# Kernel optimization log

Measured on AMD Instinct MI355X. Metric: run time of the kernel, lower is better.

## Reference

```python
import jax, jax.numpy as jnp
import numpy as np

BASIS_ORDER = 7  # basis_dim = 8 (Chebyshev T_0..T_7 of tanh(x))


def chebyshev_basis(x, order=BASIS_ORDER):
    """x: [batch, in] -> [batch, in, order+1] Chebyshev basis on tanh(x)."""
    xt = jnp.tanh(x)
    terms = [jnp.ones_like(xt), xt]
    for _ in range(2, order + 1):
        terms.append(2.0 * xt * terms[-1] - terms[-2])
    return jnp.stack(terms[: order + 1], axis=-1)


def setup_inputs() -> dict:
    key = jax.random.key(0)
    k1, k2, k3 = jax.random.split(key, 3)
    batch, in_f, out_f, K = 4096, 1024, 1024, BASIS_ORDER + 1
    x = jax.random.normal(k1, (batch, in_f), dtype=jnp.float32)
    # Kaiming-uniform-ish init scale
    bound = 1.0 / np.sqrt(in_f * K)
    weights = jax.random.uniform(k2, (out_f, in_f, K), dtype=jnp.float32,
                                 minval=-bound, maxval=bound)
    bias_param = jax.random.uniform(k3, (out_f,), dtype=jnp.float32,
                                    minval=-bound, maxval=bound)
    return {"x": x, "weights": weights, "bias_param": bias_param}


def reference(x, weights, bias_param):
    # basis: [b, i, k]; weights: [o, i, k] -> out[b, o] = sum_{i,k} basis*W
    basis = chebyshev_basis(x)  # [batch, in, K]
    out = jnp.einsum('bik,oik->bo', basis, weights)
    return out + bias_param
```

## Files before the change

### kernel.cpp

```cpp
#include <hip/hip_runtime.h>
#include <hip/hip_bf16.h>

#define MD 4096
#define ND 1024
#define KD 8192
#define IN_F 1024

typedef __bf16 bf16x8 __attribute__((ext_vector_type(8)));
typedef float f32x4 __attribute__((ext_vector_type(4)));

#define N_CONV ((ND * KD) / 8)

__global__ __launch_bounds__(256) void conv_kernel(
    const float* __restrict__ w, __bf16* __restrict__ B) {
  int j = blockIdx.x * blockDim.x + threadIdx.x;
  const float4* p = (const float4*)(w + (size_t)j * 8);
  float4 a = p[0], b = p[1];
  bf16x8 v;
  v[0] = (__bf16)a.x; v[1] = (__bf16)a.y; v[2] = (__bf16)a.z; v[3] = (__bf16)a.w;
  v[4] = (__bf16)b.x; v[5] = (__bf16)b.y; v[6] = (__bf16)b.z; v[7] = (__bf16)b.w;
  *(bf16x8*)(B + (size_t)j * 8) = v;
}

#define BM 64
#define BN 128
#define BK 64

__device__ __forceinline__ bf16x8 cheb8(float xs) {
  float ax = __builtin_fabsf(xs);
  float e = __builtin_amdgcn_exp2f(ax * 2.88539008177792681472f);
  float r = __builtin_amdgcn_rcpf(e + 1.0f);
  float t = 1.0f - 2.0f * r;
  t = __builtin_copysignf(t, xs);
  float two_t = 2.0f * t;
  float T0 = 1.0f;
  float T1 = t;
  float T2 = two_t * T1 - T0;
  float T3 = two_t * T2 - T1;
  float T4 = two_t * T3 - T2;
  float T5 = two_t * T4 - T3;
  float T6 = two_t * T5 - T4;
  float T7 = two_t * T6 - T5;
  bf16x8 v;
  v[0] = (__bf16)T0; v[1] = (__bf16)T1; v[2] = (__bf16)T2; v[3] = (__bf16)T3;
  v[4] = (__bf16)T4; v[5] = (__bf16)T5; v[6] = (__bf16)T6; v[7] = (__bf16)T7;
  return v;
}

__global__ __launch_bounds__(256) void gemm_bias(
    const float* __restrict__ x, const __bf16* __restrict__ B,
    const float* __restrict__ bias, float* __restrict__ C) {
  __shared__ __align__(16) __bf16 As[BM * BK];
  __shared__ __align__(16) __bf16 Bs[BN * BK];

  const int tid = threadIdx.x;
  const int wave = tid >> 6;
  const int lane = tid & 63;
  const int n0 = blockIdx.x * BN;
  const int m0 = blockIdx.y * BM;
  const int wm = wave >> 1;
  const int wn = wave & 1;

  const int ar = lane >> 3;
  const int swz_col = ((lane & 7) ^ ar) * 8;
  const __bf16* gB = B + (size_t)(n0 + wave * 32 + ar) * KD + swz_col;
  const __bf16* lB = Bs + (wave * 32) * BK;

  const int br = tid >> 2;
  const int bg0 = (tid & 3) * 2;
  const float* xrow = x + (size_t)(m0 + br) * IN_F + bg0;
  const int sw = br & 7;
  __bf16* aw0 = As + br * BK + ((bg0 ^ sw) * 8);
  __bf16* aw1 = As + br * BK + (((bg0 + 1) ^ sw) * 8);

  f32x4 acc[2][4];
#pragma unroll
  for (int i = 0; i < 2; i++)
#pragma unroll
    for (int j = 0; j < 4; j++) acc[i][j] = (f32x4){0.f, 0.f, 0.f, 0.f};

  const int fr = lane & 15;
  const int fr7 = fr & 7;
  const int qk = lane >> 4;

  float2 xv = *(const float2*)(xrow);

  for (int kt = 0; kt < KD; kt += BK) {
#pragma unroll
    for (int j = 0; j < 4; j++)
      __builtin_amdgcn_global_load_lds(
          (const __attribute__((address_space(1))) void*)(gB + kt + (size_t)j * 8 * KD),
          (__attribute__((address_space(3))) void*)(lB + j * 8 * BK), 16, 0, 0);

    bf16x8 v0 = cheb8(xv.x);
    bf16x8 v1 = cheb8(xv.y);
    *(bf16x8*)aw0 = v0;
    *(bf16x8*)aw1 = v1;

    if (kt + BK < KD) xv = *(const float2*)(xrow + ((kt + BK) >> 3));

    __syncthreads();

#pragma unroll
    for (int s = 0; s < 2; s++) {
      const int pa = ((s * 4 + qk) ^ fr7) * 8;
      bf16x8 af[2], bfr[4];
#pragma unroll
      for (int mi = 0; mi < 2; mi++)
        af[mi] = *(const bf16x8*)&As[(wm * 32 + mi * 16 + fr) * BK + pa];
#pragma unroll
      for (int ni = 0; ni < 4; ni++)
        bfr[ni] = *(const bf16x8*)&Bs[(wn * 64 + ni * 16 + fr) * BK + pa];
#pragma unroll
      for (int mi = 0; mi < 2; mi++)
#pragma unroll
        for (int ni = 0; ni < 4; ni++)
          acc[mi][ni] = __builtin_amdgcn_mfma_f32_16x16x32_bf16(
              af[mi], bfr[ni], acc[mi][ni], 0, 0, 0);
    }
    __syncthreads();
  }

  const int col0 = n0 + wn * 64;
  const int row0 = m0 + wm * 32 + (lane >> 4) * 4;
#pragma unroll
  for (int ni = 0; ni < 4; ni++) {
    int col = col0 + ni * 16 + (lane & 15);
    float bv = bias[col];
#pragma unroll
    for (int mi = 0; mi < 2; mi++) {
      int row = row0 + mi * 16;
#pragma unroll
      for (int r = 0; r < 4; r++)
        C[(size_t)(row + r) * ND + col] = acc[mi][ni][r] + bv;
    }
  }
}

extern "C" void kernel_launch(void* const* d_in, const int* in_sizes, int n_in,
                              void* d_out, int out_size, void* d_ws, size_t ws_size,
                              hipStream_t stream) {
  const float* x = (const float*)d_in[0];
  const float* w = (const float*)d_in[1];
  const float* bias = (const float*)d_in[2];
  float* out = (float*)d_out;

  __bf16* Bbf = (__bf16*)d_ws;

  conv_kernel<<<N_CONV / 256, 256, 0, stream>>>(w, Bbf);

  dim3 grid(ND / BN, MD / BM);
  gemm_bias<<<grid, 256, 0, stream>>>(x, Bbf, bias, out);
}
```

Baseline: 214.4 us.

## Compute A basis in registers and triple-buffer B tiles with single barrier

Drops the shared-memory A tile: each lane loads its own x values and computes the Chebyshev basis fragments directly in registers in MFMA operand layout. B tiles are triple-buffered in LDS with asynchronous global-to-LDS prefetch of the next tile, using a partial vmcnt wait and one barrier per iteration instead of two. This removes LDS traffic for A and exposes load/compute overlap, at the cost of each wave pair recomputing the basis redundantly (both wn waves compute the same A) and more LDS for B buffers. The last iteration issues a wasted prefetch of tile 0.

```diff
diff --git a/kernel.cpp b/kernel.cpp
--- a/kernel.cpp
+++ b/kernel.cpp
@@ -25,6 +25,8 @@
 #define BM 64
 #define BN 128
 #define BK 64
+#define NT (KD / BK)
+#define BUFSZ (BN * BK)
 
 __device__ __forceinline__ bf16x8 cheb8(float xs) {
   float ax = __builtin_fabsf(xs);
@@ -50,8 +52,7 @@
 __global__ __launch_bounds__(256) void gemm_bias(
     const float* __restrict__ x, const __bf16* __restrict__ B,
     const float* __restrict__ bias, float* __restrict__ C) {
-  __shared__ __align__(16) __bf16 As[BM * BK];
-  __shared__ __align__(16) __bf16 Bs[BN * BK];
+  __shared__ __align__(16) __bf16 Bs[3 * BUFSZ];
 
   const int tid = threadIdx.x;
   const int wave = tid >> 6;
@@ -64,14 +65,14 @@
   const int ar = lane >> 3;
   const int swz_col = ((lane & 7) ^ ar) * 8;
   const __bf16* gB = B + (size_t)(n0 + wave * 32 + ar) * KD + swz_col;
-  const __bf16* lB = Bs + (wave * 32) * BK;
+  const int lBoff = (wave * 32) * BK;
 
-  const int br = tid >> 2;
-  const int bg0 = (tid & 3) * 2;
-  const float* xrow = x + (size_t)(m0 + br) * IN_F + bg0;
-  const int sw = br & 7;
-  __bf16* aw0 = As + br * BK + ((bg0 ^ sw) * 8);
-  __bf16* aw1 = As + br * BK + (((bg0 + 1) ^ sw) * 8);
+  const int fr = lane & 15;
+  const int fr7 = fr & 7;
+  const int qk = lane >> 4;
+
+  const float* xr0 = x + (size_t)(m0 + wm * 32 + fr) * IN_F + qk;
+  const float* xr1 = xr0 + 16 * IN_F;
 
   f32x4 acc[2][4];
 #pragma unroll
@@ -79,46 +80,57 @@
 #pragma unroll
     for (int j = 0; j < 4; j++) acc[i][j] = (f32x4){0.f, 0.f, 0.f, 0.f};
 
-  const int fr = lane & 15;
-  const int fr7 = fr & 7;
-  const int qk = lane >> 4;
+#pragma unroll
+  for (int j = 0; j < 4; j++)
+    __builtin_amdgcn_global_load_lds(
+        (const __attribute__((address_space(1))) void*)(gB + (size_t)j * 8 * KD),
+        (__attribute__((address_space(3))) void*)(Bs + lBoff + j * 8 * BK), 16, 0, 0);
+  float xc0 = xr0[0], xc1 = xr0[4], xc2 = xr1[0], xc3 = xr1[4];
 
-  float2 xv = *(const float2*)(xrow);
+  int cur = 0, nxt = 1;
+  for (int t = 0; t < NT; ++t) {
+    const int tn = (t + 1 < NT) ? t + 1 : 0;
+    const __bf16* lB = Bs + cur * BUFSZ;
+    __bf16* sB = Bs + nxt * BUFSZ;
 
-  for (int kt = 0; kt < KD; kt += BK) {
 #pragma unroll
     for (int j = 0; j < 4; j++)
       __builtin_amdgcn_global_load_lds(
-          (const __attribute__((address_space(1))) void*)(gB + kt + (size_t)j * 8 * KD),
-          (__attribute__((address_space(3))) void*)(lB + j * 8 * BK), 16, 0, 0);
+          (const __attribute__((address_space(1))) void*)(gB + (size_t)tn * BK + (size_t)j * 8 * KD),
+          (__attribute__((address_space(3))) void*)(sB + lBoff + j * 8 * BK), 16, 0, 0);
+    float xn0 = xr0[tn * 8];
+    float xn1 = xr0[tn * 8 + 4];
+    float xn2 = xr1[tn * 8];
+    float xn3 = xr1[tn * 8 + 4];
 
-    bf16x8 v0 = cheb8(xv.x);
-    bf16x8 v1 = cheb8(xv.y);
-    *(bf16x8*)aw0 = v0;
-    *(bf16x8*)aw1 = v1;
+    asm volatile("s_waitcnt vmcnt(8)" ::: "memory");
+    __builtin_amdgcn_s_barrier();
+    __builtin_amdgcn_sched_barrier(0);
 
-    if (kt + BK < KD) xv = *(const float2*)(xrow + ((kt + BK) >> 3));
-
-    __syncthreads();
+    bf16x8 a00 = cheb8(xc0);
+    bf16x8 a01 = cheb8(xc1);
+    bf16x8 a10 = cheb8(xc2);
+    bf16x8 a11 = cheb8(xc3);
 
 #pragma unroll
     for (int s = 0; s < 2; s++) {
       const int pa = ((s * 4 + qk) ^ fr7) * 8;
-      bf16x8 af[2], bfr[4];
-#pragma unroll
-      for (int mi = 0; mi < 2; mi++)
-        af[mi] = *(const bf16x8*)&As[(wm * 32 + mi * 16 + fr) * BK + pa];
+      bf16x8 bfr[4];
 #pragma unroll
       for (int ni = 0; ni < 4; ni++)
-        bfr[ni] = *(const bf16x8*)&Bs[(wn * 64 + ni * 16 + fr) * BK + pa];
+        bfr[ni] = *(const bf16x8*)&lB[(wn * 64 + ni * 16 + fr) * BK + pa];
+      bf16x8 af0 = s ? a01 : a00;
+      bf16x8 af1 = s ? a11 : a10;
 #pragma unroll
-      for (int mi = 0; mi < 2; mi++)
-#pragma unroll
-        for (int ni = 0; ni < 4; ni++)
-          acc[mi][ni] = __builtin_amdgcn_mfma_f32_16x16x32_bf16(
-              af[mi], bfr[ni], acc[mi][ni], 0, 0, 0);
+      for (int ni = 0; ni < 4; ni++) {
+        acc[0][ni] = __builtin_amdgcn_mfma_f32_16x16x32_bf16(af0, bfr[ni], acc[0][ni], 0, 0, 0);
+        acc[1][ni] = __builtin_amdgcn_mfma_f32_16x16x32_bf16(af1, bfr[ni], acc[1][ni], 0, 0, 0);
+      }
     }
-    __syncthreads();
+
+    xc0 = xn0; xc1 = xn1; xc2 = xn2; xc3 = xn3;
+    cur = nxt;
+    nxt = (nxt == 2) ? 0 : nxt + 1;
   }
 
   const int col0 = n0 + wn * 64;
```

After: 236.5 us. 1.1x slower.

## Replace LDS-tiled GEMM with register-direct split-K waves and XCD-aware tile mapping

Applied to the files above, without the earlier changes.

Drops the shared-memory staging of A and B tiles. Each wave now loads its B fragments and x values straight from global memory into registers, prefetching one step ahead, and computes the Chebyshev basis in registers. Each block covers a 64x64 output tile with two waves that split K in half and reduce through LDS at the end. Block indices are remapped so neighbouring N tiles land on the same XCD. This removes the per-iteration barriers and LDS traffic, but loses operand sharing between waves through LDS, so global and L2 traffic goes up and each wave needs more registers.

```diff
diff --git a/kernel.cpp b/kernel.cpp
--- a/kernel.cpp
+++ b/kernel.cpp
@@ -22,10 +22,6 @@
   *(bf16x8*)(B + (size_t)j * 8) = v;
 }
 
-#define BM 64
-#define BN 128
-#define BK 64
-
 __device__ __forceinline__ bf16x8 cheb8(float xs) {
   float ax = __builtin_fabsf(xs);
   float e = __builtin_amdgcn_exp2f(ax * 2.88539008177792681472f);
@@ -47,92 +43,111 @@
   return v;
 }
 
-__global__ __launch_bounds__(256) void gemm_bias(
+__global__ __launch_bounds__(128, 2) void gemm_bias(
     const float* __restrict__ x, const __bf16* __restrict__ B,
     const float* __restrict__ bias, float* __restrict__ C) {
-  __shared__ __align__(16) __bf16 As[BM * BK];
-  __shared__ __align__(16) __bf16 Bs[BN * BK];
+  __shared__ float Cred[64][72];
 
   const int tid = threadIdx.x;
-  const int wave = tid >> 6;
+  const int w = tid >> 6;
   const int lane = tid & 63;
-  const int n0 = blockIdx.x * BN;
-  const int m0 = blockIdx.y * BM;
-  const int wm = wave >> 1;
-  const int wn = wave & 1;
+  const int fr = lane & 15;
+  const int qk = lane >> 4;
 
-  const int ar = lane >> 3;
-  const int swz_col = ((lane & 7) ^ ar) * 8;
-  const __bf16* gB = B + (size_t)(n0 + wave * 32 + ar) * KD + swz_col;
-  const __bf16* lB = Bs + (wave * 32) * BK;
+  const int bid = blockIdx.x;
+  const int xcd = bid & 7;
+  const int idx = bid >> 3;
+  const int n0 = (xcd * 2 + (idx & 1)) * 64;
+  const int m0 = (idx >> 1) * 64;
 
-  const int br = tid >> 2;
-  const int bg0 = (tid & 3) * 2;
-  const float* xrow = x + (size_t)(m0 + br) * IN_F + bg0;
-  const int sw = br & 7;
-  __bf16* aw0 = As + br * BK + ((bg0 ^ sw) * 8);
-  __bf16* aw1 = As + br * BK + (((bg0 + 1) ^ sw) * 8);
+  const __bf16* bp[4];
+#pragma unroll
+  for (int ni = 0; ni < 4; ni++)
+    bp[ni] = B + (size_t)(n0 + ni * 16 + fr) * KD + w * 4096 + qk * 8;
+  const float* xp[4];
+#pragma unroll
+  for (int mi = 0; mi < 4; mi++)
+    xp[mi] = x + (size_t)(m0 + mi * 16 + fr) * IN_F + w * 512 + qk;
 
-  f32x4 acc[2][4];
+  f32x4 acc[4][4];
 #pragma unroll
-  for (int i = 0; i < 2; i++)
+  for (int i = 0; i < 4; i++)
 #pragma unroll
     for (int j = 0; j < 4; j++) acc[i][j] = (f32x4){0.f, 0.f, 0.f, 0.f};
 
-  const int fr = lane & 15;
-  const int fr7 = fr & 7;
-  const int qk = lane >> 4;
+  bf16x8 bcur[4][2];
+  float xcur[4][2];
+#pragma unroll
+  for (int ni = 0; ni < 4; ni++) {
+    bcur[ni][0] = *(const bf16x8*)(bp[ni]);
+    bcur[ni][1] = *(const bf16x8*)(bp[ni] + 32);
+  }
+#pragma unroll
+  for (int mi = 0; mi < 4; mi++) {
+    xcur[mi][0] = xp[mi][0];
+    xcur[mi][1] = xp[mi][4];
+  }
 
-  float2 xv = *(const float2*)(xrow);
+#pragma unroll 2
+  for (int t = 0; t < 64; ++t) {
+    const int tn = (t + 1) & 63;
+    bf16x8 bnxt[4][2];
+    float xnxt[4][2];
+#pragma unroll
+    for (int ni = 0; ni < 4; ni++) {
+      bnxt[ni][0] = *(const bf16x8*)(bp[ni] + tn * 64);
+      bnxt[ni][1] = *(const bf16x8*)(bp[ni] + tn * 64 + 32);
+    }
+#pragma unroll
+    for (int mi = 0; mi < 4; mi++) {
+      xnxt[mi][0] = xp[mi][tn * 8];
+      xnxt[mi][1] = xp[mi][tn * 8 + 4];
+    }
+#pragma unroll
+    for (int mi = 0; mi < 4; mi++) {
+      bf16x8 a0 = cheb8(xcur[mi][0]);
+      bf16x8 a1 = cheb8(xcur[mi][1]);
+#pragma unroll
+      for (int ni = 0; ni < 4; ni++) {
+        acc[mi][ni] = __builtin_amdgcn_mfma_f32_16x16x32_bf16(
+            a0, bcur[ni][0], acc[mi][ni], 0, 0, 0);
+        acc[mi][ni] = __builtin_amdgcn_mfma_f32_16x16x32_bf16(
+            a1, bcur[ni][1], acc[mi][ni], 0, 0, 0);
+      }
+    }
+#pragma unroll
+    for (int ni = 0; ni < 4; ni++) {
+      bcur[ni][0] = bnxt[ni][0];
+      bcur[ni][1] = bnxt[ni][1];
+    }
+#pragma unroll
+    for (int mi = 0; mi < 4; mi++) {
+      xcur[mi][0] = xnxt[mi][0];
+      xcur[mi][1] = xnxt[mi][1];
+    }
+  }
 
-  for (int kt = 0; kt < KD; kt += BK) {
+  if (w == 1) {
 #pragma unroll
-    for (int j = 0; j < 4; j++)
-      __builtin_amdgcn_global_load_lds(
-          (const __attribute__((address_space(1))) void*)(gB + kt + (size_t)j * 8 * KD),
-          (__attribute__((address_space(3))) void*)(lB + j * 8 * BK), 16, 0, 0);
-
-    bf16x8 v0 = cheb8(xv.x);
-    bf16x8 v1 = cheb8(xv.y);
-    *(bf16x8*)aw0 = v0;
-    *(bf16x8*)aw1 = v1;
-
-    if (kt + BK < KD) xv = *(const float2*)(xrow + ((kt + BK) >> 3));
-
-    __syncthreads();
-
-#pragma unroll
-    for (int s = 0; s < 2; s++) {
-      const int pa = ((s * 4 + qk) ^ fr7) * 8;
-      bf16x8 af[2], bfr[4];
-#pragma unroll
-      for (int mi = 0; mi < 2; mi++)
-        af[mi] = *(const bf16x8*)&As[(wm * 32 + mi * 16 + fr) * BK + pa];
+    for (int mi = 0; mi < 4; mi++)
 #pragma unroll
       for (int ni = 0; ni < 4; ni++)
-        bfr[ni] = *(const bf16x8*)&Bs[(wn * 64 + ni * 16 + fr) * BK + pa];
+        *(f32x4*)&Cred[ni * 16 + fr][mi * 16 + qk * 4] = acc[mi][ni];
+  }
+  __syncthreads();
+  if (w == 0) {
 #pragma unroll
-      for (int mi = 0; mi < 2; mi++)
+    for (int ni = 0; ni < 4; ni++) {
+      const int col = n0 + ni * 16 + fr;
+      const float bv = bias[col];
 #pragma unroll
-        for (int ni = 0; ni < 4; ni++)
-          acc[mi][ni] = __builtin_amdgcn_mfma_f32_16x16x32_bf16(
-              af[mi], bfr[ni], acc[mi][ni], 0, 0, 0);
-    }
-    __syncthreads();
-  }
-
-  const int col0 = n0 + wn * 64;
-  const int row0 = m0 + wm * 32 + (lane >> 4) * 4;
+      for (int mi = 0; mi < 4; mi++) {
+        f32x4 other = *(const f32x4*)&Cred[ni * 16 + fr][mi * 16 + qk * 4];
 #pragma unroll
-  for (int ni = 0; ni < 4; ni++) {
-    int col = col0 + ni * 16 + (lane & 15);
-    float bv = bias[col];
-#pragma unroll
-    for (int mi = 0; mi < 2; mi++) {
-      int row = row0 + mi * 16;
-#pragma unroll
-      for (int r = 0; r < 4; r++)
-        C[(size_t)(row + r) * ND + col] = acc[mi][ni][r] + bv;
+        for (int r = 0; r < 4; r++)
+          C[(size_t)(m0 + mi * 16 + qk * 4 + r) * ND + col] =
+              acc[mi][ni][r] + other[r] + bv;
+      }
     }
   }
 }
@@ -149,6 +164,5 @@
 
   conv_kernel<<<N_CONV / 256, 256, 0, stream>>>(w, Bbf);
 
-  dim3 grid(ND / BN, MD / BM);
-  gemm_bias<<<grid, 256, 0, stream>>>(x, Bbf, bias, out);
+  gemm_bias<<<1024, 128, 0, stream>>>(x, Bbf, bias, out);
 }
```

Result: slower. 318.3 us (+48.5%).
